# Kernel optimization log

Hardware: AMD Instinct MI355X
Metric: run time of the kernel (lower is better)

## Reference

```python
import jax, jax.numpy as jnp
import numpy as np

B, S, D = 2, 2048, 1024
H = 16
HD = D // H  # 64


def setup_inputs() -> dict:
    key = jax.random.key(0)
    ks = jax.random.split(key, 6)
    scale = 1.0 / np.sqrt(D)
    return {
        "x": jax.random.normal(ks[0], (B, S, D), dtype=jnp.float32),
        "W_q": jax.random.normal(ks[1], (D, D), dtype=jnp.float32) * scale,
        "W_k": jax.random.normal(ks[2], (D, D), dtype=jnp.float32) * scale,
        "W_v": jax.random.normal(ks[3], (D, D), dtype=jnp.float32) * scale,
        "W_o": jax.random.normal(ks[4], (D, D), dtype=jnp.float32) * scale,
        "b_o": jax.random.normal(ks[5], (D,), dtype=jnp.float32) * 0.01,
    }


def reference(x, W_q, W_k, W_v, W_o, b_o):
    # Projections (torch Linear applies x @ W.T; weights here stored as [out, in])
    q = jnp.einsum("bsd,ed->bse", x, W_q).reshape(B, S, H, HD)
    k = jnp.einsum("bsd,ed->bse", x, W_k).reshape(B, S, H, HD)
    v = jnp.einsum("bsd,ed->bse", x, W_v).reshape(B, S, H, HD)
    # scores: [B, H, S, S]
    scores = jnp.einsum("bqhd,bkhd->bhqk", q, k) / jnp.sqrt(jnp.float32(HD))
    attn = jax.nn.softmax(scores, axis=-1)
    # dropout is identity in eval mode
    out = jnp.einsum("bhqk,bkhd->bqhd", attn, v).reshape(B, S, D)
    return jnp.einsum("bsd,ed->bse", out, W_o) + b_o
```

## Files before the change

kernel.cpp:

```cpp
#include <hip/hip_runtime.h>
#include <hip/hip_bf16.h>

typedef __hip_bfloat16 bf16_t;
typedef __bf16 bf16x8 __attribute__((ext_vector_type(8)));
typedef __bf16 bf16x4 __attribute__((ext_vector_type(4)));
typedef short  s16x4  __attribute__((ext_vector_type(4)));
typedef float  f32x4  __attribute__((ext_vector_type(4)));

#define MFMA(a, b, c) __builtin_amdgcn_mfma_f32_16x16x32_bf16((a), (b), (c), 0, 0, 0)

__device__ __forceinline__ f32x4 mfma16(bf16x4 a, bf16x4 b, f32x4 c) {
#if __has_builtin(__builtin_amdgcn_mfma_f32_16x16x16_bf16)
  return __builtin_amdgcn_mfma_f32_16x16x16_bf16(a, b, c, 0, 0, 0);
#else
  return __builtin_amdgcn_mfma_f32_16x16x16bf16_1k(
      __builtin_bit_cast(s16x4, a), __builtin_bit_cast(s16x4, b), c, 0, 0, 0);
#endif
}

__device__ __forceinline__ float fast_exp2(float x) {
#if __has_builtin(__builtin_amdgcn_exp2f)
  return __builtin_amdgcn_exp2f(x);
#else
  float r;
  asm("v_exp_f32 %0, %1" : "=v"(r) : "v"(x));
  return r;
#endif
}

__device__ __forceinline__ bf16x8 ldg8(const bf16_t* p) {
  return *reinterpret_cast<const bf16x8*>(p);
}
__device__ __forceinline__ bf16x4 ldg4(const bf16_t* p) {
  return *reinterpret_cast<const bf16x4*>(p);
}
__device__ __forceinline__ void st8(bf16_t* p, bf16x8 v) {
  *reinterpret_cast<bf16x8*>(p) = v;
}
__device__ __forceinline__ void store_out(bf16_t* p, float v) { *p = __float2bfloat16(v); }
__device__ __forceinline__ void store_out(float* p, float v)  { *p = v; }

__device__ __forceinline__ void async16(const bf16_t* g, bf16_t* l) {
  __builtin_amdgcn_global_load_lds(
      (const __attribute__((address_space(1))) void*)g,
      (__attribute__((address_space(3))) void*)l, 16, 0, 0);
}

__global__ __launch_bounds__(256) void cvt_kernel(
    const float* __restrict__ x,  const float* __restrict__ Wq,
    const float* __restrict__ Wk, const float* __restrict__ Wv,
    const float* __restrict__ Wo,
    bf16_t* __restrict__ xb,  bf16_t* __restrict__ Wqb,
    bf16_t* __restrict__ Wkb, bf16_t* __restrict__ Wvb,
    bf16_t* __restrict__ Wob) {
  const int bid = blockIdx.x;
  const float* src; bf16_t* dst; size_t base;
  float scl = 1.0f;
  if (bid < 2048)      { src = x;  dst = xb;  base = (size_t)bid * 2048; }
  else if (bid < 2560) { src = Wq; dst = Wqb; base = (size_t)(bid - 2048) * 2048;
                         scl = 0.180336878f; }
  else if (bid < 3072) { src = Wk; dst = Wkb; base = (size_t)(bid - 2560) * 2048; }
  else if (bid < 3584) { src = Wv; dst = Wvb; base = (size_t)(bid - 3072) * 2048; }
  else                 { src = Wo; dst = Wob; base = (size_t)(bid - 3584) * 2048; }
  const size_t i0 = base + (size_t)threadIdx.x * 8;
  const float4 f0 = *reinterpret_cast<const float4*>(src + i0);
  const float4 f1 = *reinterpret_cast<const float4*>(src + i0 + 4);
  bf16x8 v;
  v[0] = (__bf16)(f0.x * scl); v[1] = (__bf16)(f0.y * scl);
  v[2] = (__bf16)(f0.z * scl); v[3] = (__bf16)(f0.w * scl);
  v[4] = (__bf16)(f1.x * scl); v[5] = (__bf16)(f1.y * scl);
  v[6] = (__bf16)(f1.z * scl); v[7] = (__bf16)(f1.w * scl);
  st8(dst + i0, v);
}

#define GK 1024

template <typename OutT, bool BIAS>
__device__ __forceinline__ void gemm_tile(
    const bf16_t* __restrict__ A, const bf16_t* __restrict__ B,
    OutT* __restrict__ C, const float* __restrict__ bias,
    int bm, int bn, int ldc, bf16_t* As, bf16_t* Bs) {
  const int tid  = threadIdx.x;
  const int lane = tid & 63;
  const int wave = tid >> 6;
  const int wm   = (wave & 1) << 6;
  const int wn   = (wave >> 1) << 6;
  const int lr   = lane & 15;
  const int lq   = lane >> 4;

  const int srow = tid >> 3;
  const int sx   = ((tid & 7) ^ (srow & 7)) << 3;

  const bf16_t* Ag = A + (size_t)(bm + srow) * GK + sx;
  const bf16_t* Bg = B + (size_t)(bn + srow) * GK + sx;
  bf16_t* Asw = As + wave * 512;
  bf16_t* Bsw = Bs + wave * 512;

  f32x4 acc[4][4];
#pragma unroll
  for (int i = 0; i < 4; ++i)
#pragma unroll
    for (int j = 0; j < 4; ++j) acc[i][j] = (f32x4){0.f, 0.f, 0.f, 0.f};

  for (int k0 = 0; k0 < GK; k0 += 64) {
    __syncthreads();
#pragma unroll
    for (int g = 0; g < 4; ++g) {
      async16(Ag + k0 + (size_t)(g * 32) * GK, Asw + g * 2048);
      async16(Bg + k0 + (size_t)(g * 32) * GK, Bsw + g * 2048);
    }
    __syncthreads();
#pragma unroll
    for (int ks = 0; ks < 2; ++ks) {
      bf16x8 af[4], bf[4];
      const int chs = ((ks * 4 + lq) ^ (lr & 7)) << 3;
#pragma unroll
      for (int i = 0; i < 4; ++i) {
        af[i] = ldg8(&As[(wm + i * 16 + lr) * 64 + chs]);
        bf[i] = ldg8(&Bs[(wn + i * 16 + lr) * 64 + chs]);
      }
#pragma unroll
      for (int mi = 0; mi < 4; ++mi)
#pragma unroll
        for (int ni = 0; ni < 4; ++ni)
          acc[mi][ni] = MFMA(af[mi], bf[ni], acc[mi][ni]);
    }
  }

#pragma unroll
  for (int ni = 0; ni < 4; ++ni) {
    const int col = bn + wn + ni * 16 + lr;
    float bv = 0.f;
    if (BIAS) bv = bias[col];
#pragma unroll
    for (int mi = 0; mi < 4; ++mi) {
#pragma unroll
      for (int r = 0; r < 4; ++r) {
        const int row = bm + wm + mi * 16 + lq * 4 + r;
        store_out(&C[(size_t)row * ldc + col], acc[mi][ni][r] + bv);
      }
    }
  }
}

template <typename OutT, bool BIAS>
__device__ __forceinline__ void gemm_tile_n64(
    const bf16_t* __restrict__ A, const bf16_t* __restrict__ B,
    OutT* __restrict__ C, const float* __restrict__ bias,
    int bm, int bn, int ldc, bf16_t* As, bf16_t* Bs) {
  const int tid  = threadIdx.x;
  const int lane = tid & 63;
  const int wave = tid >> 6;
  const int wm   = (wave & 1) << 6;
  const int wn   = (wave >> 1) << 5;
  const int lr   = lane & 15;
  const int lq   = lane >> 4;

  const int srow = tid >> 3;
  const int sx   = ((tid & 7) ^ (srow & 7)) << 3;

  const bf16_t* Ag = A + (size_t)(bm + srow) * GK + sx;
  const bf16_t* Bg = B + (size_t)(bn + srow) * GK + sx;
  bf16_t* Asw = As + wave * 512;
  bf16_t* Bsw = Bs + wave * 512;

  f32x4 acc[4][2];
#pragma unroll
  for (int i = 0; i < 4; ++i)
#pragma unroll
    for (int j = 0; j < 2; ++j) acc[i][j] = (f32x4){0.f, 0.f, 0.f, 0.f};

  for (int k0 = 0; k0 < GK; k0 += 64) {
    __syncthreads();
#pragma unroll
    for (int g = 0; g < 4; ++g)
      async16(Ag + k0 + (size_t)(g * 32) * GK, Asw + g * 2048);
#pragma unroll
    for (int g = 0; g < 2; ++g)
      async16(Bg + k0 + (size_t)(g * 32) * GK, Bsw + g * 2048);
    __syncthreads();
#pragma unroll
    for (int ks = 0; ks < 2; ++ks) {
      bf16x8 af[4], bf[2];
      const int chs = ((ks * 4 + lq) ^ (lr & 7)) << 3;
#pragma unroll
      for (int i = 0; i < 4; ++i)
        af[i] = ldg8(&As[(wm + i * 16 + lr) * 64 + chs]);
#pragma unroll
      for (int i = 0; i < 2; ++i)
        bf[i] = ldg8(&Bs[(wn + i * 16 + lr) * 64 + chs]);
#pragma unroll
      for (int mi = 0; mi < 4; ++mi)
#pragma unroll
        for (int ni = 0; ni < 2; ++ni)
          acc[mi][ni] = MFMA(af[mi], bf[ni], acc[mi][ni]);
    }
  }

#pragma unroll
  for (int ni = 0; ni < 2; ++ni) {
    const int col = bn + wn + ni * 16 + lr;
    float bv = 0.f;
    if (BIAS) bv = bias[col];
#pragma unroll
    for (int mi = 0; mi < 4; ++mi) {
#pragma unroll
      for (int r = 0; r < 4; ++r) {
        const int row = bm + wm + mi * 16 + lq * 4 + r;
        store_out(&C[(size_t)row * ldc + col], acc[mi][ni][r] + bv);
      }
    }
  }
}

__global__ __launch_bounds__(256) void qkv_kernel(
    const bf16_t* __restrict__ x, const bf16_t* __restrict__ Wq,
    const bf16_t* __restrict__ Wk, const bf16_t* __restrict__ Wv,
    bf16_t* __restrict__ Q, bf16_t* __restrict__ Kp, bf16_t* __restrict__ Vt) {
  __shared__ alignas(16) bf16_t As[128 * 64];
  __shared__ alignas(16) bf16_t Bs[128 * 64];
  const int bid = blockIdx.x;
  const int z   = blockIdx.y;
  const int mt  = (bid & 31) * 128;
  const int nt  = (bid >> 5) * 128;
  if (z == 0) {
    gemm_tile<bf16_t, false>(x, Wq, Q, nullptr, mt, nt, 1024, As, Bs);
  } else if (z == 1) {
    gemm_tile<bf16_t, false>(x, Wk, Kp, nullptr, mt, nt, 1024, As, Bs);
  } else {
    gemm_tile<bf16_t, false>(Wv, x, Vt, nullptr, nt, mt, 4096, As, Bs);
  }
}

__global__ __launch_bounds__(256) void out_proj_kernel(
    const bf16_t* __restrict__ Ao, const bf16_t* __restrict__ Wo,
    const float* __restrict__ bias, float* __restrict__ out) {
  __shared__ alignas(16) bf16_t As[128 * 64];
  __shared__ alignas(16) bf16_t Bs[64 * 64];
  const int bid = blockIdx.x;
  gemm_tile_n64<float, true>(Ao, Wo, out, bias, (bid & 31) * 128,
                             (bid >> 5) * 64, 1024, As, Bs);
}

#define VPADA 132

__global__ __launch_bounds__(512, 4) void attn_kernel(
    const bf16_t* __restrict__ Q, const bf16_t* __restrict__ Kp,
    const bf16_t* __restrict__ Vt, bf16_t* __restrict__ Ao) {
  __shared__ alignas(16) char smem_raw[2 * 16384 + 2 * 16896];
  bf16_t* Ks0 = (bf16_t*)smem_raw;
  bf16_t* Ks1 = Ks0 + 8192;
  bf16_t* Vs0 = (bf16_t*)(smem_raw + 32768);
  bf16_t* Vs1 = Vs0 + 64 * VPADA;
  float*  Osc = (float*)smem_raw;

  const int tid  = threadIdx.x;
  const int lane = tid & 63;
  const int wave = tid >> 6;
  const int lr   = lane & 15;
  const int lq   = lane >> 4;
  const int bh   = blockIdx.x;
  const int qt   = blockIdx.y;
  const int b    = bh >> 4;
  const int h    = bh & 15;
  const size_t tok0 = (size_t)b * 2048;
  const int col0 = h * 64;
  const int qblk = qt * 128 + wave * 16;

  bf16x8 qf[2];
  {
    const size_t qrow = tok0 + qblk + lr;
#pragma unroll
    for (int c = 0; c < 2; ++c)
      qf[c] = ldg8(&Q[qrow * 1024 + col0 + c * 32 + lq * 8]);
  }

  f32x4 o[4];
#pragma unroll
  for (int i = 0; i < 4; ++i) o[i] = (f32x4){0.f, 0.f, 0.f, 0.f};
  float lsum = 0.f;

  const int srow = tid >> 3;
  const int sxk  = ((tid & 7) ^ (srow & 7)) << 3;
  const int sxv  = (tid & 7) << 3;
  const int kdst = wave * 512;

  const int koff0 = lr * 64 + ((lq ^ (lr & 7)) << 3);
  const int koff1 = lr * 64 + (((lq + 4) ^ (lr & 7)) << 3);
  const int voff  = lr * VPADA + lq * 4;

  const bf16_t* Kg0 = Kp + tok0 * 1024 + col0;
  const bf16_t* Vg0 = Vt + (size_t)col0 * 4096 + tok0;

  auto stage_k = [&](const bf16_t* Kg, bf16_t* Ksn) {
    async16(Kg + (size_t)srow * 1024 + sxk, Ksn + kdst);
    async16(Kg + (size_t)(srow + 64) * 1024 + sxk, Ksn + kdst + 4096);
  };

  auto compute_tile = [&](const bf16_t* Ksc, const bf16_t* Vsc) {
#pragma unroll
    for (int c = 0; c < 8; ++c) {
      const bf16x8 kf0 = ldg8(&Ksc[c * 1024 + koff0]);
      const bf16x8 kf1 = ldg8(&Ksc[c * 1024 + koff1]);
      f32x4 sT = {0.f, 0.f, 0.f, 0.f};
      sT = MFMA(kf0, qf[0], sT);
      sT = MFMA(kf1, qf[1], sT);
      const float p0 = fast_exp2(sT.x);
      const float p1 = fast_exp2(sT.y);
      const float p2 = fast_exp2(sT.z);
      const float p3 = fast_exp2(sT.w);
      bf16x4 pb;
      pb[0] = (__bf16)p0; pb[1] = (__bf16)p1;
      pb[2] = (__bf16)p2; pb[3] = (__bf16)p3;
      lsum += (p0 + p1) + (p2 + p3);
#pragma unroll
      for (int ht = 0; ht < 4; ++ht) {
        const bf16x4 vf = ldg4(&Vsc[ht * 16 * VPADA + voff + c * 16]);
        o[ht] = mfma16(vf, pb, o[ht]);
      }
    }
  };

  {
    const bf16x8 v0 = ldg8(Vg0 + (size_t)srow * 4096 + sxv);
    const bf16x8 v1 = ldg8(Vg0 + (size_t)srow * 4096 + sxv + 64);
    stage_k(Kg0, Ks0);
    st8(&Vs0[srow * VPADA + sxv], v0);
    st8(&Vs0[srow * VPADA + sxv + 64], v1);
  }

#pragma unroll 1
  for (int t = 0; t < 16; t += 2) {
    __syncthreads();
    {
      const bf16_t* Kg = Kg0 + (size_t)(t + 1) * 131072;
      const bf16_t* Vg = Vg0 + (t + 1) * 128;
      const bf16x8 v0 = ldg8(Vg + (size_t)srow * 4096 + sxv);
      const bf16x8 v1 = ldg8(Vg + (size_t)srow * 4096 + sxv + 64);
      stage_k(Kg, Ks1);
      compute_tile(Ks0, Vs0);
      st8(&Vs1[srow * VPADA + sxv], v0);
      st8(&Vs1[srow * VPADA + sxv + 64], v1);
    }
    __syncthreads();
    if (t + 2 < 16) {
      const bf16_t* Kg = Kg0 + (size_t)(t + 2) * 131072;
      const bf16_t* Vg = Vg0 + (t + 2) * 128;
      const bf16x8 v0 = ldg8(Vg + (size_t)srow * 4096 + sxv);
      const bf16x8 v1 = ldg8(Vg + (size_t)srow * 4096 + sxv + 64);
      stage_k(Kg, Ks0);
      compute_tile(Ks1, Vs1);
      st8(&Vs0[srow * VPADA + sxv], v0);
      st8(&Vs0[srow * VPADA + sxv + 64], v1);
    } else {
      compute_tile(Ks1, Vs1);
    }
  }

  __syncthreads();

  float* Ow = &Osc[wave * 64 * 17];
  {
    float ls = lsum;
    ls += __shfl_xor(ls, 16);
    ls += __shfl_xor(ls, 32);
    const float invl = 1.f / ls;

#pragma unroll
    for (int ht = 0; ht < 4; ++ht)
#pragma unroll
      for (int r = 0; r < 4; ++r)
        Ow[(ht * 16 + lq * 4 + r) * 17 + lr] = o[ht][r] * invl;

    const int qq = lane >> 2;
    const int hc = (lane & 3) * 16;
    bf16x8 w0, w1;
#pragma unroll
    for (int i = 0; i < 8; ++i) {
      w0[i] = (__bf16)Ow[(hc + i) * 17 + qq];
      w1[i] = (__bf16)Ow[(hc + 8 + i) * 17 + qq];
    }
    bf16_t* dst = Ao + (tok0 + qblk + qq) * 1024 + col0 + hc;
    st8(dst, w0);
    st8(dst + 8, w1);
  }
}

extern "C" void kernel_launch(void* const* d_in, const int* in_sizes, int n_in,
                              void* d_out, int out_size, void* d_ws, size_t ws_size,
                              hipStream_t stream) {
  const float* x  = (const float*)d_in[0];
  const float* Wq = (const float*)d_in[1];
  const float* Wk = (const float*)d_in[2];
  const float* Wv = (const float*)d_in[3];
  const float* Wo = (const float*)d_in[4];
  const float* bo = (const float*)d_in[5];
  float* out = (float*)d_out;

  const size_t NTOK = 4096, DMODEL = 1024, WSZ = DMODEL * DMODEL;
  bf16_t* xb  = (bf16_t*)d_ws;
  bf16_t* Wqb = xb + NTOK * DMODEL;
  bf16_t* Wkb = Wqb + WSZ;
  bf16_t* Wvb = Wkb + WSZ;
  bf16_t* Wob = Wvb + WSZ;
  bf16_t* Q   = Wob + WSZ;
  bf16_t* Kp  = Q  + NTOK * DMODEL;
  bf16_t* Vt  = Kp + NTOK * DMODEL;
  bf16_t* Ao  = Vt + NTOK * DMODEL;

  cvt_kernel<<<dim3(4096), 256, 0, stream>>>(x, Wq, Wk, Wv, Wo, xb, Wqb, Wkb, Wvb, Wob);
  qkv_kernel<<<dim3(256, 3), 256, 0, stream>>>(xb, Wqb, Wkb, Wvb, Q, Kp, Vt);
  attn_kernel<<<dim3(32, 16), 512, 0, stream>>>(Q, Kp, Vt, Ao);
  out_proj_kernel<<<dim3(512, 1), 256, 0, stream>>>(Ao, Wob, bo, out);
}
```

Baseline: 175.6 us.

## Triple-buffer GEMM K-loop with async LDS loads and explicit vmcnt waits

The projection GEMM tiles switch from a single-buffered 64-wide K step, synchronised with two __syncthreads per step, to a three-stage ring of 32-wide K slices. Global-to-LDS async loads for future stages are issued while the current stage is computed, and s_waitcnt vmcnt counters gate consumption. The LDS swizzle is rewritten for the 32-element row layout. This hides global memory latency behind MFMA work, but depends on the hand-set vmcnt counts and sched barriers being correct, and it halves the MFMA work between barriers.

After: 179.9 us. 2.4% more time.

```diff
diff --git a/kernel.cpp b/kernel.cpp
--- a/kernel.cpp
+++ b/kernel.cpp
@@ -45,6 +45,10 @@
       (const __attribute__((address_space(1))) void*)g,
       (__attribute__((address_space(3))) void*)l, 16, 0, 0);
 }
+
+#define VMW(n) asm volatile("s_waitcnt vmcnt(" #n ")" ::: "memory")
+#define SBAR   __builtin_amdgcn_s_barrier()
+#define SCHED0 __builtin_amdgcn_sched_barrier(0)
 
 __global__ __launch_bounds__(256) void cvt_kernel(
     const float* __restrict__ x,  const float* __restrict__ Wq,
@@ -88,13 +92,16 @@
   const int lr   = lane & 15;
   const int lq   = lane >> 4;
 
-  const int srow = tid >> 3;
-  const int sx   = ((tid & 7) ^ (srow & 7)) << 3;
-
-  const bf16_t* Ag = A + (size_t)(bm + srow) * GK + sx;
-  const bf16_t* Bg = B + (size_t)(bn + srow) * GK + sx;
-  bf16_t* Asw = As + wave * 512;
-  bf16_t* Bsw = Bs + wave * 512;
+  const int srow4 = tid >> 2;
+  const int sxc   = ((tid & 3) ^ ((srow4 >> 1) & 3)) << 3;
+
+  const bf16_t* Ag = A + (size_t)(bm + srow4) * GK + sxc;
+  const bf16_t* Bg = B + (size_t)(bn + srow4) * GK + sxc;
+  const int kdst = wave * 512;
+
+  const int rchs  = (lq ^ ((lr >> 1) & 3)) << 3;
+  const int koffA = (wm + lr) * 32 + rchs;
+  const int koffB = (wn + lr) * 32 + rchs;
 
   f32x4 acc[4][4];
 #pragma unroll
@@ -102,30 +109,45 @@
 #pragma unroll
     for (int j = 0; j < 4; ++j) acc[i][j] = (f32x4){0.f, 0.f, 0.f, 0.f};
 
-  for (int k0 = 0; k0 < GK; k0 += 64) {
-    __syncthreads();
-#pragma unroll
-    for (int g = 0; g < 4; ++g) {
-      async16(Ag + k0 + (size_t)(g * 32) * GK, Asw + g * 2048);
-      async16(Bg + k0 + (size_t)(g * 32) * GK, Bsw + g * 2048);
-    }
-    __syncthreads();
-#pragma unroll
-    for (int ks = 0; ks < 2; ++ks) {
-      bf16x8 af[4], bf[4];
-      const int chs = ((ks * 4 + lq) ^ (lr & 7)) << 3;
-#pragma unroll
-      for (int i = 0; i < 4; ++i) {
-        af[i] = ldg8(&As[(wm + i * 16 + lr) * 64 + chs]);
-        bf[i] = ldg8(&Bs[(wn + i * 16 + lr) * 64 + chs]);
-      }
-#pragma unroll
-      for (int mi = 0; mi < 4; ++mi)
-#pragma unroll
-        for (int ni = 0; ni < 4; ++ni)
-          acc[mi][ni] = MFMA(af[mi], bf[ni], acc[mi][ni]);
-    }
-  }
+  auto stage = [&](int t, bf16_t* Ap, bf16_t* Bp) {
+    const int k = t * 32;
+    async16(Ag + k, Ap + kdst);
+    async16(Ag + k + (size_t)64 * GK, Ap + kdst + 2048);
+    async16(Bg + k, Bp + kdst);
+    async16(Bg + k + (size_t)64 * GK, Bp + kdst + 2048);
+  };
+
+  auto compute = [&](const bf16_t* Ap, const bf16_t* Bp) {
+    bf16x8 af[4], bf[4];
+#pragma unroll
+    for (int i = 0; i < 4; ++i) {
+      af[i] = ldg8(&Ap[koffA + i * 512]);
+      bf[i] = ldg8(&Bp[koffB + i * 512]);
+    }
+#pragma unroll
+    for (int mi = 0; mi < 4; ++mi)
+#pragma unroll
+      for (int ni = 0; ni < 4; ++ni)
+        acc[mi][ni] = MFMA(af[mi], bf[ni], acc[mi][ni]);
+  };
+
+  bf16_t* A0 = As;          bf16_t* B0 = Bs;
+  bf16_t* A1 = As + 4096;   bf16_t* B1 = Bs + 4096;
+  bf16_t* A2 = As + 8192;   bf16_t* B2 = Bs + 8192;
+
+  stage(0, A0, B0); stage(1, A1, B1); stage(2, A2, B2);
+
+#pragma unroll 1
+  for (int t = 0; t < 27; t += 3) {
+    VMW(8); SBAR; SCHED0; compute(A0, B0); SBAR; SCHED0; stage(t + 3, A0, B0);
+    VMW(8); SBAR; SCHED0; compute(A1, B1); SBAR; SCHED0; stage(t + 4, A1, B1);
+    VMW(8); SBAR; SCHED0; compute(A2, B2); SBAR; SCHED0; stage(t + 5, A2, B2);
+  }
+  VMW(8); SBAR; SCHED0; compute(A0, B0); SBAR; SCHED0; stage(30, A0, B0);
+  VMW(8); SBAR; SCHED0; compute(A1, B1); SBAR; SCHED0; stage(31, A1, B1);
+  VMW(8); SBAR; SCHED0; compute(A2, B2);
+  VMW(4); SBAR; SCHED0; compute(A0, B0);
+  VMW(0); SBAR; SCHED0; compute(A1, B1);
 
 #pragma unroll
   for (int ni = 0; ni < 4; ++ni) {
@@ -156,13 +178,16 @@
   const int lr   = lane & 15;
   const int lq   = lane >> 4;
 
-  const int srow = tid >> 3;
-  const int sx   = ((tid & 7) ^ (srow & 7)) << 3;
-
-  const bf16_t* Ag = A + (size_t)(bm + srow) * GK + sx;
-  const bf16_t* Bg = B + (size_t)(bn + srow) * GK + sx;
-  bf16_t* Asw = As + wave * 512;
-  bf16_t* Bsw = Bs + wave * 512;
+  const int srow4 = tid >> 2;
+  const int sxc   = ((tid & 3) ^ ((srow4 >> 1) & 3)) << 3;
+
+  const bf16_t* Ag = A + (size_t)(bm + srow4) * GK + sxc;
+  const bf16_t* Bg = B + (size_t)(bn + srow4) * GK + sxc;
+  const int kdst = wave * 512;
+
+  const int rchs  = (lq ^ ((lr >> 1) & 3)) << 3;
+  const int koffA = (wm + lr) * 32 + rchs;
+  const int koffB = (wn + lr) * 32 + rchs;
 
   f32x4 acc[4][2];
 #pragma unroll
@@ -170,32 +195,45 @@
 #pragma unroll
     for (int j = 0; j < 2; ++j) acc[i][j] = (f32x4){0.f, 0.f, 0.f, 0.f};
 
-  for (int k0 = 0; k0 < GK; k0 += 64) {
-    __syncthreads();
-#pragma unroll
-    for (int g = 0; g < 4; ++g)
-      async16(Ag + k0 + (size_t)(g * 32) * GK, Asw + g * 2048);
-#pragma unroll
-    for (int g = 0; g < 2; ++g)
-      async16(Bg + k0 + (size_t)(g * 32) * GK, Bsw + g * 2048);
-    __syncthreads();
-#pragma unroll
-    for (int ks = 0; ks < 2; ++ks) {
-      bf16x8 af[4], bf[2];
-      const int chs = ((ks * 4 + lq) ^ (lr & 7)) << 3;
-#pragma unroll
-      for (int i = 0; i < 4; ++i)
-        af[i] = ldg8(&As[(wm + i * 16 + lr) * 64 + chs]);
-#pragma unroll
-      for (int i = 0; i < 2; ++i)
-        bf[i] = ldg8(&Bs[(wn + i * 16 + lr) * 64 + chs]);
-#pragma unroll
-      for (int mi = 0; mi < 4; ++mi)
-#pragma unroll
-        for (int ni = 0; ni < 2; ++ni)
-          acc[mi][ni] = MFMA(af[mi], bf[ni], acc[mi][ni]);
-    }
-  }
+  auto stage = [&](int t, bf16_t* Ap, bf16_t* Bp) {
+    const int k = t * 32;
+    async16(Ag + k, Ap + kdst);
+    async16(Ag + k + (size_t)64 * GK, Ap + kdst + 2048);
+    async16(Bg + k, Bp + kdst);
+  };
+
+  auto compute = [&](const bf16_t* Ap, const bf16_t* Bp) {
+    bf16x8 af[4], bf[2];
+#pragma unroll
+    for (int i = 0; i < 4; ++i)
+      af[i] = ldg8(&Ap[koffA + i * 512]);
+#pragma unroll
+    for (int i = 0; i < 2; ++i)
+      bf[i] = ldg8(&Bp[koffB + i * 512]);
+#pragma unroll
+    for (int mi = 0; mi < 4; ++mi)
+#pragma unroll
+      for (int ni = 0; ni < 2; ++ni)
+        acc[mi][ni] = MFMA(af[mi], bf[ni], acc[mi][ni]);
+  };
+
+  bf16_t* A0 = As;          bf16_t* B0 = Bs;
+  bf16_t* A1 = As + 4096;   bf16_t* B1 = Bs + 2048;
+  bf16_t* A2 = As + 8192;   bf16_t* B2 = Bs + 4096;
+
+  stage(0, A0, B0); stage(1, A1, B1); stage(2, A2, B2);
+
+#pragma unroll 1
+  for (int t = 0; t < 27; t += 3) {
+    VMW(6); SBAR; SCHED0; compute(A0, B0); SBAR; SCHED0; stage(t + 3, A0, B0);
+    VMW(6); SBAR; SCHED0; compute(A1, B1); SBAR; SCHED0; stage(t + 4, A1, B1);
+    VMW(6); SBAR; SCHED0; compute(A2, B2); SBAR; SCHED0; stage(t + 5, A2, B2);
+  }
+  VMW(6); SBAR; SCHED0; compute(A0, B0); SBAR; SCHED0; stage(30, A0, B0);
+  VMW(6); SBAR; SCHED0; compute(A1, B1); SBAR; SCHED0; stage(31, A1, B1);
+  VMW(6); SBAR; SCHED0; compute(A2, B2);
+  VMW(3); SBAR; SCHED0; compute(A0, B0);
+  VMW(0); SBAR; SCHED0; compute(A1, B1);
 
 #pragma unroll
   for (int ni = 0; ni < 2; ++ni) {
@@ -217,8 +255,8 @@
     const bf16_t* __restrict__ x, const bf16_t* __restrict__ Wq,
     const bf16_t* __restrict__ Wk, const bf16_t* __restrict__ Wv,
     bf16_t* __restrict__ Q, bf16_t* __restrict__ Kp, bf16_t* __restrict__ Vt) {
-  __shared__ alignas(16) bf16_t As[128 * 64];
-  __shared__ alignas(16) bf16_t Bs[128 * 64];
+  __shared__ alignas(16) bf16_t As[3 * 128 * 32];
+  __shared__ alignas(16) bf16_t Bs[3 * 128 * 32];
   const int bid = blockIdx.x;
   const int z   = blockIdx.y;
   const int mt  = (bid & 31) * 128;
@@ -235,8 +273,8 @@
 __global__ __launch_bounds__(256) void out_proj_kernel(
     const bf16_t* __restrict__ Ao, const bf16_t* __restrict__ Wo,
     const float* __restrict__ bias, float* __restrict__ out) {
-  __shared__ alignas(16) bf16_t As[128 * 64];
-  __shared__ alignas(16) bf16_t Bs[64 * 64];
+  __shared__ alignas(16) bf16_t As[3 * 128 * 32];
+  __shared__ alignas(16) bf16_t Bs[3 * 64 * 32];
   const int bid = blockIdx.x;
   gemm_tile_n64<float, true>(Ao, Wo, out, bias, (bid & 31) * 128,
                              (bid >> 5) * 64, 1024, As, Bs);
```

## Split KV tile across wave pairs with two query subtiles per wave

Applied to the files above, without the earlier changes.

Each wave now processes 32 query rows (two 16-row subtiles) over half of each 128-key tile, with waves 0-3 and 4-7 splitting the key chunks. Each K and V fragment read from shared memory now feeds two MFMAs, which cuts LDS traffic per FLOP. The two halves' partial outputs and row sums are combined through shared memory at the end. In exchange it adds a cross-wave reduction step and an extra barrier, and raises register pressure from doubled accumulators under launch_bounds(512,4).

Result: slower. 192.6 us (+9.7%).

```diff
diff --git a/kernel.cpp b/kernel.cpp
--- a/kernel.cpp
+++ b/kernel.cpp
@@ -252,11 +252,12 @@
   bf16_t* Ks1 = Ks0 + 8192;
   bf16_t* Vs0 = (bf16_t*)(smem_raw + 32768);
   bf16_t* Vs1 = Vs0 + 64 * VPADA;
-  float*  Osc = (float*)smem_raw;
 
   const int tid  = threadIdx.x;
   const int lane = tid & 63;
   const int wave = tid >> 6;
+  const int wq   = wave & 3;
+  const int kvh  = wave >> 2;
   const int lr   = lane & 15;
   const int lq   = lane >> 4;
   const int bh   = blockIdx.x;
@@ -265,20 +266,23 @@
   const int h    = bh & 15;
   const size_t tok0 = (size_t)b * 2048;
   const int col0 = h * 64;
-  const int qblk = qt * 128 + wave * 16;
-
-  bf16x8 qf[2];
-  {
-    const size_t qrow = tok0 + qblk + lr;
+  const int qblk = qt * 128 + wq * 32;
+
+  bf16x8 qf[2][2];
+#pragma unroll
+  for (int nt = 0; nt < 2; ++nt) {
+    const size_t qrow = tok0 + qblk + nt * 16 + lr;
 #pragma unroll
     for (int c = 0; c < 2; ++c)
-      qf[c] = ldg8(&Q[qrow * 1024 + col0 + c * 32 + lq * 8]);
-  }
-
-  f32x4 o[4];
-#pragma unroll
-  for (int i = 0; i < 4; ++i) o[i] = (f32x4){0.f, 0.f, 0.f, 0.f};
-  float lsum = 0.f;
+      qf[nt][c] = ldg8(&Q[qrow * 1024 + col0 + c * 32 + lq * 8]);
+  }
+
+  f32x4 o[2][4];
+#pragma unroll
+  for (int nt = 0; nt < 2; ++nt)
+#pragma unroll
+    for (int i = 0; i < 4; ++i) o[nt][i] = (f32x4){0.f, 0.f, 0.f, 0.f};
+  float lsum[2] = {0.f, 0.f};
 
   const int srow = tid >> 3;
   const int sxk  = ((tid & 7) ^ (srow & 7)) << 3;
@@ -288,6 +292,7 @@
   const int koff0 = lr * 64 + ((lq ^ (lr & 7)) << 3);
   const int koff1 = lr * 64 + (((lq + 4) ^ (lr & 7)) << 3);
   const int voff  = lr * VPADA + lq * 4;
+  const int c0    = kvh * 4;
 
   const bf16_t* Kg0 = Kp + tok0 * 1024 + col0;
   const bf16_t* Vg0 = Vt + (size_t)col0 * 4096 + tok0;
@@ -299,24 +304,29 @@
 
   auto compute_tile = [&](const bf16_t* Ksc, const bf16_t* Vsc) {
 #pragma unroll
-    for (int c = 0; c < 8; ++c) {
+    for (int cc = 0; cc < 4; ++cc) {
+      const int c = c0 + cc;
       const bf16x8 kf0 = ldg8(&Ksc[c * 1024 + koff0]);
       const bf16x8 kf1 = ldg8(&Ksc[c * 1024 + koff1]);
-      f32x4 sT = {0.f, 0.f, 0.f, 0.f};
-      sT = MFMA(kf0, qf[0], sT);
-      sT = MFMA(kf1, qf[1], sT);
-      const float p0 = fast_exp2(sT.x);
-      const float p1 = fast_exp2(sT.y);
-      const float p2 = fast_exp2(sT.z);
-      const float p3 = fast_exp2(sT.w);
-      bf16x4 pb;
-      pb[0] = (__bf16)p0; pb[1] = (__bf16)p1;
-      pb[2] = (__bf16)p2; pb[3] = (__bf16)p3;
-      lsum += (p0 + p1) + (p2 + p3);
+      bf16x4 pb[2];
+#pragma unroll
+      for (int nt = 0; nt < 2; ++nt) {
+        f32x4 sT = {0.f, 0.f, 0.f, 0.f};
+        sT = MFMA(kf0, qf[nt][0], sT);
+        sT = MFMA(kf1, qf[nt][1], sT);
+        const float p0 = fast_exp2(sT.x);
+        const float p1 = fast_exp2(sT.y);
+        const float p2 = fast_exp2(sT.z);
+        const float p3 = fast_exp2(sT.w);
+        pb[nt][0] = (__bf16)p0; pb[nt][1] = (__bf16)p1;
+        pb[nt][2] = (__bf16)p2; pb[nt][3] = (__bf16)p3;
+        lsum[nt] += (p0 + p1) + (p2 + p3);
+      }
 #pragma unroll
       for (int ht = 0; ht < 4; ++ht) {
         const bf16x4 vf = ldg4(&Vsc[ht * 16 * VPADA + voff + c * 16]);
-        o[ht] = mfma16(vf, pb, o[ht]);
+        o[0][ht] = mfma16(vf, pb[0], o[0][ht]);
+        o[1][ht] = mfma16(vf, pb[1], o[1][ht]);
       }
     }
   };
@@ -359,30 +369,62 @@
 
   __syncthreads();
 
-  float* Ow = &Osc[wave * 64 * 17];
-  {
-    float ls = lsum;
-    ls += __shfl_xor(ls, 16);
-    ls += __shfl_xor(ls, 32);
-    const float invl = 1.f / ls;
-
-#pragma unroll
-    for (int ht = 0; ht < 4; ++ht)
-#pragma unroll
-      for (int r = 0; r < 4; ++r)
-        Ow[(ht * 16 + lq * 4 + r) * 17 + lr] = o[ht][r] * invl;
-
-    const int qq = lane >> 2;
-    const int hc = (lane & 3) * 16;
-    bf16x8 w0, w1;
-#pragma unroll
-    for (int i = 0; i < 8; ++i) {
-      w0[i] = (__bf16)Ow[(hc + i) * 17 + qq];
-      w1[i] = (__bf16)Ow[(hc + 8 + i) * 17 + qq];
-    }
-    bf16_t* dst = Ao + (tok0 + qblk + qq) * 1024 + col0 + hc;
-    st8(dst, w0);
-    st8(dst + 8, w1);
+  float ls[2];
+#pragma unroll
+  for (int nt = 0; nt < 2; ++nt) {
+    float v = lsum[nt];
+    v += __shfl_xor(v, 16);
+    v += __shfl_xor(v, 32);
+    ls[nt] = v;
+  }
+
+  float* Pex = (float*)smem_raw;
+  float* lex = (float*)(smem_raw + 32768);
+  float* Osc = (float*)(smem_raw + 33280);
+
+  if (kvh == 1) {
+#pragma unroll
+    for (int nt = 0; nt < 2; ++nt) {
+      float* P = Pex + (wq * 2 + nt) * 1024;
+#pragma unroll
+      for (int ht = 0; ht < 4; ++ht)
+#pragma unroll
+        for (int r = 0; r < 4; ++r)
+          P[(ht * 16 + lq * 4 + r) * 16 + lr] = o[nt][ht][r];
+      if (lq == 0) lex[(wq * 2 + nt) * 16 + lr] = ls[nt];
+    }
+  }
+  __syncthreads();
+  if (kvh == 0) {
+    float* Ow = Osc + wq * 1088;
+#pragma unroll
+    for (int nt = 0; nt < 2; ++nt) {
+      const float* P = Pex + (wq * 2 + nt) * 1024;
+#pragma unroll
+      for (int ht = 0; ht < 4; ++ht)
+#pragma unroll
+        for (int r = 0; r < 4; ++r)
+          o[nt][ht][r] += P[(ht * 16 + lq * 4 + r) * 16 + lr];
+      const float invl = 1.f / (ls[nt] + lex[(wq * 2 + nt) * 16 + lr]);
+
+#pragma unroll
+      for (int ht = 0; ht < 4; ++ht)
+#pragma unroll
+        for (int r = 0; r < 4; ++r)
+          Ow[(ht * 16 + lq * 4 + r) * 17 + lr] = o[nt][ht][r] * invl;
+
+      const int qq = lane >> 2;
+      const int hc = (lane & 3) * 16;
+      bf16x8 w0, w1;
+#pragma unroll
+      for (int i = 0; i < 8; ++i) {
+        w0[i] = (__bf16)Ow[(hc + i) * 17 + qq];
+        w1[i] = (__bf16)Ow[(hc + 8 + i) * 17 + qq];
+      }
+      bf16_t* dst = Ao + (tok0 + qblk + nt * 16 + qq) * 1024 + col0 + hc;
+      st8(dst, w0);
+      st8(dst + 8, w1);
+    }
   }
 }
 
```
